# Optimization experiments

Hardware: AMD Instinct MI355X
Metric: run time of the kernel (lower is better)

## Reference

```python
import jax, jax.numpy as jnp
import numpy as np

EPS = 1e-5

def _layer_norm(x, g, b):
    mu = jnp.mean(x, axis=-1, keepdims=True)
    var = jnp.mean(jnp.square(x - mu), axis=-1, keepdims=True)
    return (x - mu) * jax.lax.rsqrt(var + EPS) * g + b

def setup_inputs() -> dict:
    key = jax.random.key(0)
    ks = jax.random.split(key, 8)
    B, S, H, NH, FF = 2, 2048, 2048, 16, 8192
    x = jax.random.normal(ks[0], (B, S, H), dtype=jnp.float32)
    # causal mask: True = masked (matches masked_fill semantics)
    mask = jnp.triu(jnp.ones((S, S), dtype=bool), k=1)
    sc = 0.02
    wq = jax.random.normal(ks[1], (H, H), dtype=jnp.float32) * sc
    wk = jax.random.normal(ks[2], (H, H), dtype=jnp.float32) * sc
    wv = jax.random.normal(ks[3], (H, H), dtype=jnp.float32) * sc
    wo = jax.random.normal(ks[4], (H, H), dtype=jnp.float32) * sc
    w_in = jax.random.normal(ks[5], (H, FF), dtype=jnp.float32) * sc
    w_out = jax.random.normal(ks[6], (FF, H), dtype=jnp.float32) * sc
    ln1_g = jnp.ones((H,), jnp.float32); ln1_b = jnp.zeros((H,), jnp.float32)
    ln2_g = jnp.ones((H,), jnp.float32); ln2_b = jnp.zeros((H,), jnp.float32)
    return {"x": x, "mask": mask, "wq": wq, "wk": wk, "wv": wv, "wo": wo,
            "w_in": w_in, "w_out": w_out,
            "ln1_g": ln1_g, "ln1_b": ln1_b, "ln2_g": ln2_g, "ln2_b": ln2_b}

def reference(x, mask, wq, wk, wv, wo, w_in, w_out, ln1_g, ln1_b, ln2_g, ln2_b):
    B, S, H = x.shape
    NH = 16
    HD = H // NH
    scale = HD ** (-0.5)
    # attention with pre-norm
    xn = _layer_norm(x, ln1_g, ln1_b)
    q = (xn @ wq).reshape(B, S, NH, HD)
    k = (xn @ wk).reshape(B, S, NH, HD)
    v = (xn @ wv).reshape(B, S, NH, HD)
    scores = jnp.einsum('bqhd,bkhd->bhqk', q, k) * scale
    scores = jnp.where(mask[:S, :S], -jnp.inf, scores)
    attn = jax.nn.softmax(scores, axis=-1)
    out = jnp.einsum('bhqk,bkhd->bqhd', attn, v).reshape(B, S, H)
    h = x + out @ wo
    # FFN with pre-norm, tanh-approx GELU
    hn = _layer_norm(h, ln2_g, ln2_b)
    ff = jax.nn.gelu(hn @ w_in, approximate=True) @ w_out
    return h + ff
```

## Files before the change

kernel.cpp:

```cpp
#include <hip/hip_runtime.h>
#include <hip/hip_bf16.h>

#define B_ 2
#define S_ 2048
#define H_ 2048
#define NH_ 16
#define HD_ 128
#define FF_ 8192

typedef __attribute__((ext_vector_type(8))) short bf16x8;
typedef __attribute__((ext_vector_type(4))) float f32x4;

#define NEG_BIG (-1e30f)

#define GLL16(gp, lp)                                                                    \
  __builtin_amdgcn_global_load_lds((const __attribute__((address_space(1))) void*)(gp),  \
                                   (__attribute__((address_space(3))) void*)(lp), 16, 0, 0)

__device__ __forceinline__ float b2f(unsigned short u) {
  union { unsigned int i; float f; } c; c.i = ((unsigned int)u) << 16; return c.f;
}
__device__ __forceinline__ unsigned short f2b(float f) {
  unsigned int u = __float_as_uint(f);
  u += 0x7fffu + ((u >> 16) & 1u);
  return (unsigned short)(u >> 16);
}
__device__ __forceinline__ float ldf(const void* p, size_t i, int f32) {
  return f32 ? ((const float*)p)[i] : b2f(((const unsigned short*)p)[i]);
}
__device__ __forceinline__ void unpack8(uint4 r, float* f) {
  f[0] = b2f((unsigned short)(r.x & 0xffffu)); f[1] = b2f((unsigned short)(r.x >> 16));
  f[2] = b2f((unsigned short)(r.y & 0xffffu)); f[3] = b2f((unsigned short)(r.y >> 16));
  f[4] = b2f((unsigned short)(r.z & 0xffffu)); f[5] = b2f((unsigned short)(r.z >> 16));
  f[6] = b2f((unsigned short)(r.w & 0xffffu)); f[7] = b2f((unsigned short)(r.w >> 16));
}

__global__ void detect_k(const unsigned int* __restrict__ x, int* __restrict__ flagp) {
  if (threadIdx.x == 0) {
    int c = 0;
    for (int i = 0; i < 256; ++i) {
      unsigned int e = (x[i] >> 7) & 0xffu;
      c += (e >= 97u && e <= 130u) ? 1 : 0;
    }
    *flagp = (c < 128) ? 1 : 0;
  }
}

__global__ __launch_bounds__(256) void transpose_k(const void* __restrict__ in,
                                                   unsigned short* __restrict__ out,
                                                   int R, int C,
                                                   const int* __restrict__ flagp) {
  __shared__ unsigned short tile[32][33];
  int f32 = *flagp;
  int r0 = blockIdx.y * 32, c0 = blockIdx.x * 32;
  int tx = threadIdx.x & 31, ty = threadIdx.x >> 5;
#pragma unroll
  for (int p = 0; p < 4; ++p)
    tile[ty + p * 8][tx] = f2b(ldf(in, (size_t)(r0 + ty + p * 8) * C + c0 + tx, f32));
  __syncthreads();
#pragma unroll
  for (int p = 0; p < 4; ++p)
    out[(size_t)(c0 + ty + p * 8) * R + r0 + tx] = tile[tx][ty + p * 8];
}

__global__ __launch_bounds__(256) void v_transpose_k(const unsigned short* __restrict__ qkv,
                                                     unsigned short* __restrict__ VT) {
  __shared__ unsigned short tile[32][33];
  int bh = blockIdx.z;
  int b = bh >> 4, h = bh & 15;
  int s0 = blockIdx.x * 32, d0 = blockIdx.y * 32;
  int tx = threadIdx.x & 31, ty = threadIdx.x >> 5;
#pragma unroll
  for (int p = 0; p < 4; ++p) {
    int s = s0 + ty + p * 8;
    tile[ty + p * 8][tx] = qkv[(size_t)(b * S_ + s) * (3 * H_) + 2 * H_ + h * HD_ + d0 + tx];
  }
  __syncthreads();
#pragma unroll
  for (int p = 0; p < 4; ++p)
    VT[((size_t)bh * HD_ + d0 + ty + p * 8) * S_ + s0 + tx] = tile[tx][ty + p * 8];
}

__global__ __launch_bounds__(256) void ln_k(const void* __restrict__ x,
                                            const void* __restrict__ g,
                                            const void* __restrict__ b,
                                            unsigned short* __restrict__ y,
                                            const int* __restrict__ flagp, int in_mode) {
  __shared__ float red[2][4];
  int f32 = *flagp;
  int xf = in_mode ? f32 : 0;
  int row = blockIdx.x;
  int t = threadIdx.x;
  float v[8];
  size_t base = (size_t)row * H_ + t * 8;
  if (xf) {
    const float4* p = reinterpret_cast<const float4*>((const float*)x + base);
    float4 u0 = p[0], u1 = p[1];
    v[0] = u0.x; v[1] = u0.y; v[2] = u0.z; v[3] = u0.w;
    v[4] = u1.x; v[5] = u1.y; v[6] = u1.z; v[7] = u1.w;
  } else {
    unpack8(*reinterpret_cast<const uint4*>((const unsigned short*)x + base), v);
  }
  float s1 = 0.f, s2 = 0.f;
#pragma unroll
  for (int i = 0; i < 8; ++i) { s1 += v[i]; s2 += v[i] * v[i]; }
#pragma unroll
  for (int off = 32; off > 0; off >>= 1) {
    s1 += __shfl_down(s1, off);
    s2 += __shfl_down(s2, off);
  }
  int w = t >> 6, lane = t & 63;
  if (lane == 0) { red[0][w] = s1; red[1][w] = s2; }
  __syncthreads();
  s1 = red[0][0] + red[0][1] + red[0][2] + red[0][3];
  s2 = red[1][0] + red[1][1] + red[1][2] + red[1][3];
  float mu = s1 * (1.0f / H_);
  float var = s2 * (1.0f / H_) - mu * mu;
  float rinv = rsqrtf(var + 1e-5f);
  float gv[8], bv[8];
#pragma unroll
  for (int i = 0; i < 8; ++i) {
    gv[i] = ldf(g, t * 8 + i, f32);
    bv[i] = ldf(b, t * 8 + i, f32);
  }
  unsigned int o[4];
#pragma unroll
  for (int i = 0; i < 4; ++i) {
    unsigned short lo = f2b((v[2 * i] - mu) * rinv * gv[2 * i] + bv[2 * i]);
    unsigned short hi = f2b((v[2 * i + 1] - mu) * rinv * gv[2 * i + 1] + bv[2 * i + 1]);
    o[i] = (unsigned int)lo | ((unsigned int)hi << 16);
  }
  uint4 ov; ov.x = o[0]; ov.y = o[1]; ov.z = o[2]; ov.w = o[3];
  *reinterpret_cast<uint4*>(y + base) = ov;
}

#define PH_BAR() do { asm volatile("" ::: "memory"); __builtin_amdgcn_s_barrier(); \
                      asm volatile("" ::: "memory"); } while (0)
#define VMC(n) asm volatile("s_waitcnt vmcnt(" #n ")" ::: "memory")

#define STA(buf_, h_, kt_) do {                                                        \
  GLL16(pA0 + (size_t)(h_) * 128 * K + (kt_) * 64, &LdsA[buf_][(h_) * 8192 + lw]);     \
  GLL16(pA1 + (size_t)(h_) * 128 * K + (kt_) * 64, &LdsA[buf_][(h_) * 8192 + 4096 + lw]); } while (0)
#define STB(buf_, h_, kt_) do {                                                        \
  GLL16(pB0 + (size_t)(h_) * 128 * K + (kt_) * 64, &LdsB[buf_][(h_) * 8192 + lw]);     \
  GLL16(pB1 + (size_t)(h_) * 128 * K + (kt_) * 64, &LdsB[buf_][(h_) * 8192 + 4096 + lw]); } while (0)

#define LDA4(AF, buf_, mb_) do { _Pragma("unroll")                                     \
  for (int mi_ = 0; mi_ < 4; ++mi_) {                                                  \
    const unsigned short* _p = &LdsA[buf_][(wr * 128 + ((mb_) + mi_) * 16 + l15) * 64];\
    AF[mi_][0] = *reinterpret_cast<const bf16x8*>(_p + cs0);                           \
    AF[mi_][1] = *reinterpret_cast<const bf16x8*>(_p + cs1); } } while (0)
#define LDB2(BF, buf_, nb_) do { _Pragma("unroll")                                     \
  for (int ni_ = 0; ni_ < 2; ++ni_) {                                                  \
    const unsigned short* _p = &LdsB[buf_][(wc * 64 + ((nb_) + ni_) * 16 + l15) * 64]; \
    BF[ni_][0] = *reinterpret_cast<const bf16x8*>(_p + cs0);                           \
    BF[ni_][1] = *reinterpret_cast<const bf16x8*>(_p + cs1); } } while (0)

#define MF8(AF, BF, MO, NO) do { _Pragma("unroll")                                     \
  for (int mi_ = 0; mi_ < 4; ++mi_) { _Pragma("unroll")                                \
    for (int ni_ = 0; ni_ < 2; ++ni_) {                                                \
      acc[(MO) + mi_][(NO) + ni_] = __builtin_amdgcn_mfma_f32_16x16x32_bf16(           \
          AF[mi_][0], BF[ni_][0], acc[(MO) + mi_][(NO) + ni_], 0, 0, 0);               \
      acc[(MO) + mi_][(NO) + ni_] = __builtin_amdgcn_mfma_f32_16x16x32_bf16(           \
          AF[mi_][1], BF[ni_][1], acc[(MO) + mi_][(NO) + ni_], 0, 0, 0);               \
    } } } while (0)

#define GITER(LAST, tO, tE2, tO2) do {                                                 \
                                                                              \
  LDA4(aL, 0, 0); LDB2(bL, 0, 0);                                                      \
  STA(1, 1, tO);                                                                       \
  PH_BAR(); __builtin_amdgcn_s_setprio(1);                                             \
  MF8(aL, bL, 0, 0);                                                                   \
  __builtin_amdgcn_s_setprio(0);                                                       \
                                                                              \
  LDB2(bH, 0, 2);                                                                      \
  PH_BAR(); __builtin_amdgcn_s_setprio(1);                                             \
  MF8(aL, bH, 0, 2);                                                                   \
  __builtin_amdgcn_s_setprio(0);                                                       \
                                                                              \
  LDA4(aH, 0, 4);                                                                      \
  if (!(LAST)) STB(0, 0, tE2);                                                         \
  PH_BAR(); __builtin_amdgcn_s_setprio(1);                                             \
  MF8(aH, bL, 4, 0);                                                                   \
  __builtin_amdgcn_s_setprio(0);                                                       \
                                                                              \
  if (!(LAST)) { STB(0, 1, tE2); STA(0, 0, tE2); VMC(6); } else { VMC(0); }            \
  PH_BAR(); __builtin_amdgcn_s_setprio(1);                                             \
  MF8(aH, bH, 4, 2);                                                                   \
  __builtin_amdgcn_s_setprio(0);                                                       \
                                                                              \
  LDA4(aL, 1, 0); LDB2(bL, 1, 0);                                                      \
  if (!(LAST)) STA(0, 1, tE2);                                                         \
  PH_BAR(); __builtin_amdgcn_s_setprio(1);                                             \
  MF8(aL, bL, 0, 0);                                                                   \
  __builtin_amdgcn_s_setprio(0);                                                       \
                                                                              \
  LDB2(bH, 1, 2);                                                                      \
  PH_BAR(); __builtin_amdgcn_s_setprio(1);                                             \
  MF8(aL, bH, 0, 2);                                                                   \
  __builtin_amdgcn_s_setprio(0);                                                       \
                                                                              \
  LDA4(aH, 1, 4);                                                                      \
  if (!(LAST)) STB(1, 0, tO2);                                                         \
  PH_BAR(); __builtin_amdgcn_s_setprio(1);                                             \
  MF8(aH, bL, 4, 0);                                                                   \
  __builtin_amdgcn_s_setprio(0);                                                       \
                                                                              \
  if (!(LAST)) { STB(1, 1, tO2); STA(1, 0, tO2); VMC(6); }                             \
  PH_BAR(); __builtin_amdgcn_s_setprio(1);                                             \
  MF8(aH, bH, 4, 2);                                                                   \
  __builtin_amdgcn_s_setprio(0);                                                       \
} while (0)

template <int EPI>
__global__ __launch_bounds__(512) void gemm256(const unsigned short* __restrict__ A,
                                               const unsigned short* __restrict__ BT,
                                               void* __restrict__ C,
                                               const void* __restrict__ resid,
                                               int M, int N, int K,
                                               const int* __restrict__ flagp,
                                               int resid_mode, int store_mode, int nbx,
                                               int nxy, int Klen,
                                               size_t pslice, int prow) {
  (void)M;
  __shared__ unsigned short LdsA[2][16384];
  __shared__ unsigned short LdsB[2][16384];

  unsigned nwg = gridDim.x, q = nwg >> 3;
  unsigned o = blockIdx.x;
  unsigned wg = (o & 7u) * q + (o >> 3);
  int ks = 0;
  if (nxy) { ks = (int)(wg / (unsigned)nxy); wg -= (unsigned)ks * (unsigned)nxy; }
  int bx = (int)(wg % (unsigned)nbx), by = (int)(wg / (unsigned)nbx);
  int m_base = by * 256, n_base = bx * 256;
  size_t koff = (size_t)ks * (size_t)Klen;

  int tid = threadIdx.x;
  int w = tid >> 6, lane = tid & 63;
  int l15 = lane & 15, quad = lane >> 4;
  int wr = w >> 2, wc = w & 3;

  int row0 = w * 8 + (lane >> 3);
  int scb  = (lane & 7) ^ (lane >> 3);
  const unsigned short* pA0 = A + (size_t)(m_base + row0) * K + koff + scb * 8;
  const unsigned short* pA1 = pA0 + (size_t)64 * K;
  const unsigned short* pB0 = BT + (size_t)(n_base + row0) * K + koff + scb * 8;
  const unsigned short* pB1 = pB0 + (size_t)64 * K;
  unsigned lw = (unsigned)w * 512;

  int cs0 = ((quad) ^ (l15 & 7)) * 8;
  int cs1 = ((4 + quad) ^ (l15 & 7)) * 8;

  f32x4 acc[8][4];
#pragma unroll
  for (int i = 0; i < 8; ++i)
#pragma unroll
    for (int j = 0; j < 4; ++j) acc[i][j] = (f32x4){0.f, 0.f, 0.f, 0.f};

  bf16x8 aL[4][2], aH[4][2], bL[2][2], bH[2][2];

  STA(0, 0, 0); STA(0, 1, 0); STB(0, 0, 0); STB(0, 1, 0);
  STB(1, 0, 1); STB(1, 1, 1); STA(1, 0, 1);
  VMC(6);
  PH_BAR();

  int niter = Klen >> 7;
  for (int i = 0; i < niter - 1; ++i) GITER(0, 2 * i + 1, 2 * i + 2, 2 * i + 3);
  GITER(1, 2 * niter - 1, 0, 0);

  int f32 = 0, rf = 0, sf = 0;
  if (EPI != 3) {
    f32 = *flagp;
    rf = resid_mode ? f32 : 0;
    sf = store_mode ? f32 : 0;
  }
#pragma unroll
  for (int mi = 0; mi < 8; ++mi) {
#pragma unroll
    for (int ni = 0; ni < 4; ++ni) {
#pragma unroll
      for (int r = 0; r < 4; ++r) {
        int row = m_base + wr * 128 + mi * 16 + quad * 4 + r;
        int col = n_base + wc * 64 + ni * 16 + l15;
        float v = acc[mi][ni][r];
        if (EPI == 3) {
          ((float*)C)[(size_t)ks * pslice + (size_t)row * prow + col] = v;
        } else {
          size_t idx = (size_t)row * N + col;
          if (EPI == 1) v += ldf(resid, idx, rf);
          if (EPI == 2) {
            float u = v;
            float tt = 0.7978845608028654f * (u + 0.044715f * u * u * u);
            tt = fminf(tt, 15.0f);
            float s = __expf(2.0f * tt);
            v = u * s / (s + 1.0f);
          }
          if (sf) ((float*)C)[idx] = v;
          else    ((unsigned short*)C)[idx] = f2b(v);
        }
      }
    }
  }
}

__global__ __launch_bounds__(256) void red_k(const float* __restrict__ P,
                                             void* __restrict__ out,
                                             const void* __restrict__ resid,
                                             int prow, size_t pslice,
                                             const int* __restrict__ flagp,
                                             int resid_mode, int store_mode) {
  int f32 = *flagp;
  int rf = resid_mode ? f32 : 0;
  int sf = store_mode ? f32 : 0;
  size_t gid = (size_t)blockIdx.x * 256 + threadIdx.x;
  int r = (int)(gid >> 8);
  int c = ((int)gid & 255) * 8;
  size_t pb = (size_t)r * prow + c;
  const float4* p0 = reinterpret_cast<const float4*>(P + pb);
  const float4* p1 = reinterpret_cast<const float4*>(P + pslice + pb);
  float4 a0 = p0[0], a1 = p0[1];
  float4 b0 = p1[0], b1 = p1[1];
  float v[8] = {a0.x + b0.x, a0.y + b0.y, a0.z + b0.z, a0.w + b0.w,
                a1.x + b1.x, a1.y + b1.y, a1.z + b1.z, a1.w + b1.w};
  size_t ob = (size_t)r * 2048 + c;
  if (rf) {
    const float4* rp = reinterpret_cast<const float4*>((const float*)resid + ob);
    float4 r0 = rp[0], r1 = rp[1];
    v[0] += r0.x; v[1] += r0.y; v[2] += r0.z; v[3] += r0.w;
    v[4] += r1.x; v[5] += r1.y; v[6] += r1.z; v[7] += r1.w;
  } else {
    float rr[8];
    unpack8(*reinterpret_cast<const uint4*>((const unsigned short*)resid + ob), rr);
#pragma unroll
    for (int j = 0; j < 8; ++j) v[j] += rr[j];
  }
  if (sf) {
    float4 s0 = {v[0], v[1], v[2], v[3]}, s1 = {v[4], v[5], v[6], v[7]};
    float4* op = reinterpret_cast<float4*>((float*)out + ob);
    op[0] = s0; op[1] = s1;
  } else {
    unsigned int oo[4];
#pragma unroll
    for (int i = 0; i < 4; ++i)
      oo[i] = (unsigned int)f2b(v[2 * i]) | ((unsigned int)f2b(v[2 * i + 1]) << 16);
    uint4 ov; ov.x = oo[0]; ov.y = oo[1]; ov.z = oo[2]; ov.w = oo[3];
    *reinterpret_cast<uint4*>((unsigned short*)out + ob) = ov;
  }
}

__global__ __launch_bounds__(256) void attn_k(const unsigned short* __restrict__ qkv,
                                              const unsigned short* __restrict__ VT,
                                              unsigned short* __restrict__ out) {
  __shared__ unsigned short Ks[64 * 128];
  __shared__ unsigned short Vs[128 * 64];
  __shared__ unsigned short Ps[4][16][72];
  int qb = blockIdx.x, bh = blockIdx.y;
  int b = bh >> 4, h = bh & 15;
  int q0 = qb * 64;
  int tid = threadIdx.x;
  int w = tid >> 6, lane = tid & 63, l15 = lane & 15, quad = lane >> 4;
  const float scale = 0.08838834764831845f;

  bf16x8 aq[4];
  {
    const unsigned short* qrow =
        qkv + (size_t)(b * S_ + q0 + w * 16 + l15) * (3 * H_) + h * HD_;
#pragma unroll
    for (int ks = 0; ks < 4; ++ks)
      aq[ks] = *reinterpret_cast<const bf16x8*>(qrow + ks * 32 + quad * 8);
  }

  int krow_off = lane >> 4;
  int kcb = lane & 15;
  int vrow_off = lane >> 3;
  int vcb = lane & 7;

  f32x4 o[8];
#pragma unroll
  for (int f = 0; f < 8; ++f) o[f] = (f32x4){0.f, 0.f, 0.f, 0.f};
  float m_i[4], l_i[4];
#pragma unroll
  for (int r = 0; r < 4; ++r) { m_i[r] = NEG_BIG; l_i[r] = 0.f; }

  const unsigned short* kbase = qkv + (size_t)b * S_ * (3 * H_) + H_ + h * HD_;
  const unsigned short* vbase = VT + (size_t)bh * HD_ * S_;

  for (int kv0 = 0; kv0 <= q0; kv0 += 64) {
    __syncthreads();
#pragma unroll
    for (int t = 0; t < 4; ++t) {
      int krow = w * 16 + t * 4 + krow_off;
      int kswz = kcb ^ (krow & 7);
      GLL16(kbase + (size_t)(kv0 + krow) * (3 * H_) + kswz * 8, &Ks[(w * 16 + t * 4) * 128]);
      int vrow = w * 32 + t * 8 + vrow_off;
      int vswz = vcb ^ (vrow & 7);
      GLL16(vbase + (size_t)vrow * S_ + kv0 + vswz * 8, &Vs[(w * 32 + t * 8) * 64]);
    }
    __syncthreads();

    f32x4 sc[4];
#pragma unroll
    for (int j = 0; j < 4; ++j) sc[j] = (f32x4){0.f, 0.f, 0.f, 0.f};
#pragma unroll
    for (int ks = 0; ks < 4; ++ks) {
#pragma unroll
      for (int j = 0; j < 4; ++j) {
        int r = j * 16 + l15;
        bf16x8 bk = *reinterpret_cast<const bf16x8*>(
            &Ks[r * 128 + (((ks * 4 + quad) ^ (l15 & 7))) * 8]);
        sc[j] = __builtin_amdgcn_mfma_f32_16x16x32_bf16(aq[ks], bk, sc[j], 0, 0, 0);
      }
    }
    bool diag = (kv0 == q0);
#pragma unroll
    for (int j = 0; j < 4; ++j)
#pragma unroll
      for (int r = 0; r < 4; ++r) {
        float s = sc[j][r] * scale;
        if (diag && (j * 16 + l15 > w * 16 + quad * 4 + r)) s = NEG_BIG;
        sc[j][r] = s;
      }

    float mx[4];
#pragma unroll
    for (int r = 0; r < 4; ++r) {
      mx[r] = sc[0][r];
#pragma unroll
      for (int j = 1; j < 4; ++j) mx[r] = fmaxf(mx[r], sc[j][r]);
    }
#pragma unroll
    for (int mm = 1; mm <= 8; mm <<= 1)
#pragma unroll
      for (int r = 0; r < 4; ++r) mx[r] = fmaxf(mx[r], __shfl_xor(mx[r], mm));
    float alpha[4];
#pragma unroll
    for (int r = 0; r < 4; ++r) {
      float mn = fmaxf(m_i[r], mx[r]);
      alpha[r] = __expf(m_i[r] - mn);
      m_i[r] = mn;
    }
    float pr[4][4], rs[4] = {0.f, 0.f, 0.f, 0.f};
#pragma unroll
    for (int j = 0; j < 4; ++j)
#pragma unroll
      for (int r = 0; r < 4; ++r) {
        float p = __expf(sc[j][r] - m_i[r]);
        pr[j][r] = p;
        rs[r] += p;
      }
#pragma unroll
    for (int mm = 1; mm <= 8; mm <<= 1)
#pragma unroll
      for (int r = 0; r < 4; ++r) rs[r] += __shfl_xor(rs[r], mm);
#pragma unroll
    for (int r = 0; r < 4; ++r) l_i[r] = l_i[r] * alpha[r] + rs[r];
#pragma unroll
    for (int f = 0; f < 8; ++f)
#pragma unroll
      for (int r = 0; r < 4; ++r) o[f][r] *= alpha[r];

#pragma unroll
    for (int j = 0; j < 4; ++j)
#pragma unroll
      for (int r = 0; r < 4; ++r)
        Ps[w][quad * 4 + r][j * 16 + l15] = f2b(pr[j][r]);

#pragma unroll
    for (int ks2 = 0; ks2 < 2; ++ks2) {
      bf16x8 ap = *reinterpret_cast<const bf16x8*>(&Ps[w][l15][ks2 * 32 + quad * 8]);
#pragma unroll
      for (int f = 0; f < 8; ++f) {
        int r = f * 16 + l15;
        bf16x8 bv = *reinterpret_cast<const bf16x8*>(
            &Vs[r * 64 + (((ks2 * 4 + quad) ^ (l15 & 7))) * 8]);
        o[f] = __builtin_amdgcn_mfma_f32_16x16x32_bf16(ap, bv, o[f], 0, 0, 0);
      }
    }
  }

  float inv[4];
#pragma unroll
  for (int r = 0; r < 4; ++r) inv[r] = 1.0f / l_i[r];
#pragma unroll
  for (int f = 0; f < 8; ++f)
#pragma unroll
    for (int r = 0; r < 4; ++r)
      out[(size_t)(b * S_ + q0 + w * 16 + quad * 4 + r) * H_ + h * HD_ + f * 16 + l15] =
          f2b(o[f][r] * inv[r]);
}

extern "C" void kernel_launch(void* const* d_in, const int* in_sizes, int n_in,
                              void* d_out, int out_size, void* d_ws, size_t ws_size,
                              hipStream_t stream) {
  (void)in_sizes; (void)n_in; (void)out_size; (void)ws_size;
  const void* x     = d_in[0];
  const void* wq    = d_in[2];
  const void* wk    = d_in[3];
  const void* wv    = d_in[4];
  const void* wo    = d_in[5];
  const void* w_in  = d_in[6];
  const void* w_out = d_in[7];
  const void* g1    = d_in[8];
  const void* b1    = d_in[9];
  const void* g2    = d_in[10];
  const void* b2    = d_in[11];
  char* ws = (char*)d_ws;

  const size_t MB = 1024 * 1024;
  unsigned short* W  = (unsigned short*)(ws + 0 * MB);
  unsigned short* E  = (unsigned short*)(ws + 32 * MB);
  unsigned short* F  = (unsigned short*)(ws + 48 * MB);
  unsigned short* Hb = (unsigned short*)(ws + 112 * MB);
  int* flagp         = (int*)(ws + 128 * MB);

  unsigned short* wqkvT = W;
  unsigned short* xn    = E;
  unsigned short* qkv   = F;
  unsigned short* VT    = F + (size_t)B_ * S_ * 3 * H_;
  unsigned short* attnb = E;
  unsigned short* hbuf  = Hb;
  unsigned short* hn    = E;
  unsigned short* ff1   = F;
  float*          Pop   = (float*)F;

  dim3 blk(256);
  dim3 gblk(512);
  detect_k<<<1, 64, 0, stream>>>((const unsigned int*)x, flagp);
  transpose_k<<<dim3(H_ / 32, H_ / 32), blk, 0, stream>>>(wq, wqkvT, H_, H_, flagp);
  transpose_k<<<dim3(H_ / 32, H_ / 32), blk, 0, stream>>>(wk, wqkvT + (size_t)H_ * H_, H_, H_, flagp);
  transpose_k<<<dim3(H_ / 32, H_ / 32), blk, 0, stream>>>(wv, wqkvT + (size_t)2 * H_ * H_, H_, H_, flagp);
  ln_k<<<B_ * S_, blk, 0, stream>>>(x, g1, b1, xn, flagp, 1);
  gemm256<0><<<dim3((3 * H_ / 256) * (B_ * S_ / 256)), gblk, 0, stream>>>(
      xn, wqkvT, qkv, nullptr, B_ * S_, 3 * H_, H_, flagp, 0, 0, 3 * H_ / 256,
      0, H_, 0, 0);
  v_transpose_k<<<dim3(S_ / 32, HD_ / 32, B_ * NH_), blk, 0, stream>>>(qkv, VT);
  attn_k<<<dim3(S_ / 64, B_ * NH_), blk, 0, stream>>>(qkv, VT, attnb);
  transpose_k<<<dim3(H_ / 32, H_ / 32), blk, 0, stream>>>(wo, W, H_, H_, flagp);
  gemm256<3><<<dim3(2 * (H_ / 256) * (B_ * S_ / 256)), gblk, 0, stream>>>(
      attnb, W, (void*)Pop, nullptr, B_ * S_, H_, H_, flagp, 0, 0, H_ / 256,
      (H_ / 256) * (B_ * S_ / 256), H_ / 2, (size_t)B_ * S_ * H_, H_);
  red_k<<<dim3((B_ * S_ * H_) / (256 * 8)), blk, 0, stream>>>(
      Pop, hbuf, x, H_, (size_t)B_ * S_ * H_, flagp, 1, 0);
  ln_k<<<B_ * S_, blk, 0, stream>>>(hbuf, g2, b2, hn, flagp, 0);
  transpose_k<<<dim3(FF_ / 32, H_ / 32), blk, 0, stream>>>(w_in, W, H_, FF_, flagp);
  gemm256<2><<<dim3((FF_ / 256) * (B_ * S_ / 256)), gblk, 0, stream>>>(
      hn, W, ff1, nullptr, B_ * S_, FF_, H_, flagp, 0, 0, FF_ / 256,
      0, H_, 0, 0);
  transpose_k<<<dim3(H_ / 32, FF_ / 32), blk, 0, stream>>>(w_out, W, FF_, H_, flagp);
  gemm256<3><<<dim3(2 * (H_ / 256) * (B_ * S_ / 256)), gblk, 0, stream>>>(
      ff1, W, (void*)ff1, nullptr, B_ * S_, H_, FF_, flagp, 0, 0, H_ / 256,
      (H_ / 256) * (B_ * S_ / 256), FF_ / 2, (size_t)H_, 2 * H_);
  red_k<<<dim3((B_ * S_ * H_) / (256 * 8)), blk, 0, stream>>>(
      (const float*)ff1, d_out, hbuf, 2 * H_, (size_t)H_, flagp, 0, 1);
}
```

Measured before the change: 985.1 us.

## Double-buffer K/V tiles in attention and remap grid for XCD locality and causal balance

The attention kernel now keeps two LDS buffers for K and V. It issues the global-to-LDS loads for the next KV tile before computing on the current one, which cuts the two barriers per iteration to one. The launch grid becomes 1D, mapped so each XCD serves fixed heads for L2 reuse, with the longest causal query blocks scheduled first for better load balance. The cost is doubled LDS for K/V, which may lower occupancy, and the overlap depends on the barrier draining the async loads.

```diff
diff --git a/kernel.cpp b/kernel.cpp
--- a/kernel.cpp
+++ b/kernel.cpp
@@ -351,10 +351,13 @@
 __global__ __launch_bounds__(256) void attn_k(const unsigned short* __restrict__ qkv,
                                               const unsigned short* __restrict__ VT,
                                               unsigned short* __restrict__ out) {
-  __shared__ unsigned short Ks[64 * 128];
-  __shared__ unsigned short Vs[128 * 64];
+  __shared__ unsigned short Ks[2][64 * 128];
+  __shared__ unsigned short Vs[2][128 * 64];
   __shared__ unsigned short Ps[4][16][72];
-  int qb = blockIdx.x, bh = blockIdx.y;
+  unsigned o = blockIdx.x;
+  int xcd = (int)(o & 7u), j = (int)(o >> 3);
+  int bh = xcd + 8 * (j >> 5);
+  int qb = 31 - (j & 31);
   int b = bh >> 4, h = bh & 15;
   int q0 = qb * 64;
   int tid = threadIdx.x;
@@ -375,9 +378,9 @@
   int vrow_off = lane >> 3;
   int vcb = lane & 7;
 
-  f32x4 o[8];
-#pragma unroll
-  for (int f = 0; f < 8; ++f) o[f] = (f32x4){0.f, 0.f, 0.f, 0.f};
+  f32x4 o_[8];
+#pragma unroll
+  for (int f = 0; f < 8; ++f) o_[f] = (f32x4){0.f, 0.f, 0.f, 0.f};
   float m_i[4], l_i[4];
 #pragma unroll
   for (int r = 0; r < 4; ++r) { m_i[r] = NEG_BIG; l_i[r] = 0.f; }
@@ -385,40 +388,47 @@
   const unsigned short* kbase = qkv + (size_t)b * S_ * (3 * H_) + H_ + h * HD_;
   const unsigned short* vbase = VT + (size_t)bh * HD_ * S_;
 
-  for (int kv0 = 0; kv0 <= q0; kv0 += 64) {
-    __syncthreads();
-#pragma unroll
-    for (int t = 0; t < 4; ++t) {
-      int krow = w * 16 + t * 4 + krow_off;
-      int kswz = kcb ^ (krow & 7);
-      GLL16(kbase + (size_t)(kv0 + krow) * (3 * H_) + kswz * 8, &Ks[(w * 16 + t * 4) * 128]);
-      int vrow = w * 32 + t * 8 + vrow_off;
-      int vswz = vcb ^ (vrow & 7);
-      GLL16(vbase + (size_t)vrow * S_ + kv0 + vswz * 8, &Vs[(w * 32 + t * 8) * 64]);
-    }
-    __syncthreads();
+#define ATTN_STAGE(buf_, kv0_) do {                                                     \
+  _Pragma("unroll")                                                                     \
+  for (int t = 0; t < 4; ++t) {                                                         \
+    int krow = w * 16 + t * 4 + krow_off;                                               \
+    int ksz = kcb ^ (krow & 7);                                                         \
+    GLL16(kbase + (size_t)((kv0_) + krow) * (3 * H_) + ksz * 8,                         \
+          &Ks[buf_][(w * 16 + t * 4) * 128]);                                           \
+    int vrow = w * 32 + t * 8 + vrow_off;                                               \
+    int vsz = vcb ^ (vrow & 7);                                                         \
+    GLL16(vbase + (size_t)vrow * S_ + (kv0_) + vsz * 8,                                 \
+          &Vs[buf_][(w * 32 + t * 8) * 64]);                                            \
+  } } while (0)
+
+  ATTN_STAGE(0, 0);
+  __syncthreads();
+
+  int cur = 0;
+  for (int kv0 = 0; kv0 <= q0; kv0 += 64, cur ^= 1) {
+    if (kv0 + 64 <= q0) ATTN_STAGE(cur ^ 1, kv0 + 64);
 
     f32x4 sc[4];
 #pragma unroll
-    for (int j = 0; j < 4; ++j) sc[j] = (f32x4){0.f, 0.f, 0.f, 0.f};
+    for (int jj = 0; jj < 4; ++jj) sc[jj] = (f32x4){0.f, 0.f, 0.f, 0.f};
 #pragma unroll
     for (int ks = 0; ks < 4; ++ks) {
 #pragma unroll
-      for (int j = 0; j < 4; ++j) {
-        int r = j * 16 + l15;
+      for (int jj = 0; jj < 4; ++jj) {
+        int r = jj * 16 + l15;
         bf16x8 bk = *reinterpret_cast<const bf16x8*>(
-            &Ks[r * 128 + (((ks * 4 + quad) ^ (l15 & 7))) * 8]);
-        sc[j] = __builtin_amdgcn_mfma_f32_16x16x32_bf16(aq[ks], bk, sc[j], 0, 0, 0);
+            &Ks[cur][r * 128 + (((ks * 4 + quad) ^ (l15 & 7))) * 8]);
+        sc[jj] = __builtin_amdgcn_mfma_f32_16x16x32_bf16(aq[ks], bk, sc[jj], 0, 0, 0);
       }
     }
     bool diag = (kv0 == q0);
 #pragma unroll
-    for (int j = 0; j < 4; ++j)
+    for (int jj = 0; jj < 4; ++jj)
 #pragma unroll
       for (int r = 0; r < 4; ++r) {
-        float s = sc[j][r] * scale;
-        if (diag && (j * 16 + l15 > w * 16 + quad * 4 + r)) s = NEG_BIG;
-        sc[j][r] = s;
+        float s = sc[jj][r] * scale;
+        if (diag && (jj * 16 + l15 > w * 16 + quad * 4 + r)) s = NEG_BIG;
+        sc[jj][r] = s;
       }
 
     float mx[4];
@@ -426,7 +436,7 @@
     for (int r = 0; r < 4; ++r) {
       mx[r] = sc[0][r];
 #pragma unroll
-      for (int j = 1; j < 4; ++j) mx[r] = fmaxf(mx[r], sc[j][r]);
+      for (int jj = 1; jj < 4; ++jj) mx[r] = fmaxf(mx[r], sc[jj][r]);
     }
 #pragma unroll
     for (int mm = 1; mm <= 8; mm <<= 1)
@@ -441,11 +451,11 @@
     }
     float pr[4][4], rs[4] = {0.f, 0.f, 0.f, 0.f};
 #pragma unroll
-    for (int j = 0; j < 4; ++j)
+    for (int jj = 0; jj < 4; ++jj)
 #pragma unroll
       for (int r = 0; r < 4; ++r) {
-        float p = __expf(sc[j][r] - m_i[r]);
-        pr[j][r] = p;
+        float p = __expf(sc[jj][r] - m_i[r]);
+        pr[jj][r] = p;
         rs[r] += p;
       }
 #pragma unroll
@@ -457,13 +467,13 @@
 #pragma unroll
     for (int f = 0; f < 8; ++f)
 #pragma unroll
-      for (int r = 0; r < 4; ++r) o[f][r] *= alpha[r];
-
-#pragma unroll
-    for (int j = 0; j < 4; ++j)
+      for (int r = 0; r < 4; ++r) o_[f][r] *= alpha[r];
+
+#pragma unroll
+    for (int jj = 0; jj < 4; ++jj)
 #pragma unroll
       for (int r = 0; r < 4; ++r)
-        Ps[w][quad * 4 + r][j * 16 + l15] = f2b(pr[j][r]);
+        Ps[w][quad * 4 + r][jj * 16 + l15] = f2b(pr[jj][r]);
 
 #pragma unroll
     for (int ks2 = 0; ks2 < 2; ++ks2) {
@@ -472,10 +482,12 @@
       for (int f = 0; f < 8; ++f) {
         int r = f * 16 + l15;
         bf16x8 bv = *reinterpret_cast<const bf16x8*>(
-            &Vs[r * 64 + (((ks2 * 4 + quad) ^ (l15 & 7))) * 8]);
-        o[f] = __builtin_amdgcn_mfma_f32_16x16x32_bf16(ap, bv, o[f], 0, 0, 0);
+            &Vs[cur][r * 64 + (((ks2 * 4 + quad) ^ (l15 & 7))) * 8]);
+        o_[f] = __builtin_amdgcn_mfma_f32_16x16x32_bf16(ap, bv, o_[f], 0, 0, 0);
       }
     }
+
+    __syncthreads();
   }
 
   float inv[4];
@@ -486,7 +498,7 @@
 #pragma unroll
     for (int r = 0; r < 4; ++r)
       out[(size_t)(b * S_ + q0 + w * 16 + quad * 4 + r) * H_ + h * HD_ + f * 16 + l15] =
-          f2b(o[f][r] * inv[r]);
+          f2b(o_[f][r] * inv[r]);
 }
 
 extern "C" void kernel_launch(void* const* d_in, const int* in_sizes, int n_in,
@@ -534,7 +546,7 @@
       xn, wqkvT, qkv, nullptr, B_ * S_, 3 * H_, H_, flagp, 0, 0, 3 * H_ / 256,
       0, H_, 0, 0);
   v_transpose_k<<<dim3(S_ / 32, HD_ / 32, B_ * NH_), blk, 0, stream>>>(qkv, VT);
-  attn_k<<<dim3(S_ / 64, B_ * NH_), blk, 0, stream>>>(qkv, VT, attnb);
+  attn_k<<<dim3(S_ / 64 * B_ * NH_), blk, 0, stream>>>(qkv, VT, attnb);
   transpose_k<<<dim3(H_ / 32, H_ / 32), blk, 0, stream>>>(wo, W, H_, H_, flagp);
   gemm256<3><<<dim3(2 * (H_ / 256) * (B_ * S_ / 256)), gblk, 0, stream>>>(
       attnb, W, (void*)Pop, nullptr, B_ * S_, H_, H_, flagp, 0, 0, H_ / 256,
```

Measured after the change: 920.0 us. 6.6% less time.
